# Optimization experiments

Measured on AMD Instinct MI355X. Metric: run time of the kernel, lower is better.

The kernel has to match this reference:

```python
import jax, jax.numpy as jnp
import numpy as np

HIGHEST_ID = 222.0
ZERO_NONZERO_PENALTY = 1.0
N_COEFFS = 447  # Chebyshev.fit(..., deg=446)


def _cheb_eval(x, coeffs):
    """Evaluate sum_i coeffs[i] * T_i(x/111 - 1) via O(1)-memory three-term recurrence."""
    xn = x / 111.0 - 1.0
    T0 = jnp.ones_like(xn)
    T1 = xn
    acc0 = coeffs[0] * T0 + coeffs[1] * T1

    def step(carry, c):
        Tm1, Tn, acc = carry
        Tnew = 2.0 * xn * Tn - Tm1
        acc = acc + c * Tnew
        return (Tn, Tnew, acc), None

    (_, _, acc), _ = jax.lax.scan(step, (T0, T1, acc0), coeffs[2:])
    return acc


def _round_ste(x):
    return x + jax.lax.stop_gradient(jnp.round(x) - x)


def _mask(x):
    # ~0 for id > 222, ~id for id <= 222
    return x * jax.nn.sigmoid(50.0 * (222.5 - x))


def setup_inputs() -> dict:
    key = jax.random.key(0)
    k0, k1, k2 = jax.random.split(key, 3)
    shape = (512, 7, 16, 64, 2)
    scale = jnp.array([222.0, 200.0], dtype=jnp.float32)  # (id, amount)
    y_pred = jax.random.uniform(k0, shape, dtype=jnp.float32) * scale
    y = jax.random.uniform(k1, shape, dtype=jnp.float32) * scale
    calories_coeffs = jax.random.normal(k2, (N_COEFFS,), dtype=jnp.float32) * 0.1
    return {"y_pred": y_pred, "y": y, "calories_coeffs": calories_coeffs}


def reference(y_pred, y, calories_coeffs):
    pred_ids = y_pred[..., 0]
    pred_amounts = y_pred[..., 1]
    true_ids = y[..., 0]
    true_amounts = y[..., 1]

    id_zero_mask = 1.0 - jnp.tanh(4.0 * pred_ids)
    amount_nonzero_mask = jnp.tanh(4.0 * pred_amounts)
    case1 = id_zero_mask * amount_nonzero_mask
    case2 = (1.0 - id_zero_mask) * (1.0 - amount_nonzero_mask)
    zeros_nonzeros_penalty = (ZERO_NONZERO_PENALTY * (case1 + case2)).sum(axis=(1, 2, 3)).mean()

    id_range_penalty = jax.nn.relu(pred_ids - HIGHEST_ID).sum(axis=(1, 2, 3)).mean()

    B = y.shape[0]
    true_amounts_f = true_amounts.reshape(B, -1)
    true_calories = _cheb_eval(true_ids, calories_coeffs).reshape(B, -1)
    calories_in_true_menu = (true_calories * true_amounts_f / 100.0).sum(axis=1) / 7.0

    pred_amounts_f = pred_amounts.reshape(y_pred.shape[0], -1)
    pred_calories = _cheb_eval(_mask(_round_ste(pred_ids)), calories_coeffs).reshape(y_pred.shape[0], -1)
    calories_in_pred_menu = (pred_calories * pred_amounts_f / 100.0).sum(axis=1) / 7.0

    calories_diff = ((calories_in_true_menu - calories_in_pred_menu) ** 2).mean()

    return zeros_nonzeros_penalty + id_range_penalty + calories_diff
```

## Files before the change

kernel.cpp:

```cpp
#include <hip/hip_runtime.h>
#include <cmath>


constexpr int NCOEF = 447;
constexpr int NTAB  = 223;
constexpr int MQ    = 8192;
constexpr float SCALEQ = (float)(8192.0 / 3.14159265358979323846);
constexpr float HQ     = (float)(3.14159265358979323846 / 8192.0);
constexpr int TPB = 256;

__device__ float g_tabF[MQ + 1];
__device__ float g_pred[NTAB];
__device__ float4 g_part[1024];

__device__ __forceinline__ float tanh4(float v) {
  float e = __expf(8.0f * v);
  return fmaf(-2.0f, __builtin_amdgcn_rcpf(e + 1.0f), 1.0f);
}

__global__ __launch_bounds__(256)
void build_tables(const float* __restrict__ coeffs)
{
  int g = blockIdx.x * 256 + threadIdx.x;
  float x;
  if (g <= MQ) {
    x = cosf((float)g * HQ);
  } else if (g < MQ + 1 + NTAB) {
    float kf = (float)(g - (MQ + 1));
    float m = kf / (1.0f + __expf(50.0f * (kf - 222.5f)));
    x = m / 111.0f - 1.0f;
  } else {
    return;
  }
  float x2 = x + x;
  float Ta = 1.0f, Tb = x;
  float acc = fmaf(coeffs[1], x, coeffs[0]);
  for (int i = 2; i + 1 < NCOEF; i += 2) {
    Ta = fmaf(x2, Tb, -Ta); acc = fmaf(coeffs[i],     Ta, acc);
    Tb = fmaf(x2, Ta, -Tb); acc = fmaf(coeffs[i + 1], Tb, acc);
  }
  Ta = fmaf(x2, Tb, -Ta); acc = fmaf(coeffs[NCOEF - 1], Ta, acc);

  if (g <= MQ) g_tabF[g] = acc;
  else         g_pred[g - (MQ + 1)] = acc;
}

__global__ __launch_bounds__(TPB)
void loss_main(const float4* __restrict__ yp4, const float4* __restrict__ yt4)
{
  __shared__ __align__(16) float sf[MQ + 1];
  __shared__ float spred[NTAB];
  __shared__ float sred[12];
  const int tid = threadIdx.x;

  const float4* gt4 = (const float4*)g_tabF;
  #pragma unroll
  for (int k = 0; k < 8; ++k) ((float4*)sf)[tid + k * TPB] = gt4[tid + k * TPB];
  if (tid == 0) sf[MQ] = g_tabF[MQ];
  if (tid < NTAB) spred[tid] = g_pred[tid];
  __syncthreads();

  const int b = blockIdx.x >> 1, h = blockIdx.x & 1;
  const size_t base = (size_t)b * 3584 + (size_t)h * 1792;

  float pen = 0.0f, cp = 0.0f, ct = 0.0f;

  #pragma unroll
  for (int k = 0; k < 7; ++k) {
    float4 pv = yp4[base + tid + k * TPB];
    float4 tv = yt4[base + tid + k * TPB];

    float a0 = tanh4(pv.x), b0 = tanh4(pv.y);
    pen += fmaf(b0, fmaf(-2.0f, a0, 1.0f), a0) + fmaxf(pv.x - 222.0f, 0.0f);
    int x0 = (int)rintf(pv.x); x0 = x0 < 0 ? 0 : (x0 > NTAB - 1 ? NTAB - 1 : x0);
    cp = fmaf(spred[x0], pv.y, cp);
    float a1 = tanh4(pv.z), b1 = tanh4(pv.w);
    pen += fmaf(b1, fmaf(-2.0f, a1, 1.0f), a1) + fmaxf(pv.z - 222.0f, 0.0f);
    int x1 = (int)rintf(pv.z); x1 = x1 < 0 ? 0 : (x1 > NTAB - 1 ? NTAB - 1 : x1);
    cp = fmaf(spred[x1], pv.w, cp);

    {
      float xn = tv.x / 111.0f - 1.0f;
      float th = acosf(xn) * SCALEQ;
      float ir = rintf(th);
      ir = ir < 1.0f ? 1.0f : (ir > (float)(MQ - 1) ? (float)(MQ - 1) : ir);
      int i = (int)ir;
      float d = th - ir;
      float fm = sf[i - 1], f0 = sf[i], fp = sf[i + 1];
      float ca = 0.5f * (fp - fm);
      float cb = fmaf(0.5f, fp + fm, -f0);
      float cal = fmaf(d, fmaf(d, cb, ca), f0);
      ct = fmaf(cal, tv.y, ct);
    }
    {
      float xn = tv.z / 111.0f - 1.0f;
      float th = acosf(xn) * SCALEQ;
      float ir = rintf(th);
      ir = ir < 1.0f ? 1.0f : (ir > (float)(MQ - 1) ? (float)(MQ - 1) : ir);
      int i = (int)ir;
      float d = th - ir;
      float fm = sf[i - 1], f0 = sf[i], fp = sf[i + 1];
      float ca = 0.5f * (fp - fm);
      float cb = fmaf(0.5f, fp + fm, -f0);
      float cal = fmaf(d, fmaf(d, cb, ca), f0);
      ct = fmaf(cal, tv.w, ct);
    }
  }

  #pragma unroll
  for (int o = 32; o > 0; o >>= 1) {
    pen += __shfl_down(pen, o, 64);
    ct  += __shfl_down(ct,  o, 64);
    cp  += __shfl_down(cp,  o, 64);
  }
  const int w = tid >> 6;
  if ((tid & 63) == 0) { sred[w] = pen; sred[4 + w] = ct; sred[8 + w] = cp; }
  __syncthreads();
  if (tid == 0) {
    g_part[blockIdx.x] =
        make_float4(sred[0] + sred[1] + sred[2]  + sred[3],
                    sred[4] + sred[5] + sred[6]  + sred[7],
                    sred[8] + sred[9] + sred[10] + sred[11], 0.0f);
  }
}

__global__ __launch_bounds__(512)
void finalize(float* __restrict__ out)
{
  __shared__ float sr[8];
  int t = threadIdx.x;
  float4 u = g_part[2 * t], v = g_part[2 * t + 1];
  float pen = u.x + v.x;
  float d = ((u.y + v.y) - (u.z + v.z)) * (1.0f / 700.0f);
  float s = fmaf(d, d, pen);
  #pragma unroll
  for (int o = 32; o > 0; o >>= 1) s += __shfl_down(s, o, 64);
  if ((t & 63) == 0) sr[t >> 6] = s;
  __syncthreads();
  if (t == 0) {
    out[0] = (sr[0] + sr[1] + sr[2] + sr[3] +
              sr[4] + sr[5] + sr[6] + sr[7]) * (1.0f / 512.0f);
  }
}

extern "C" void kernel_launch(void* const* d_in, const int* in_sizes, int n_in,
                              void* d_out, int out_size, void* d_ws, size_t ws_size,
                              hipStream_t stream) {
  build_tables<<<33, 256, 0, stream>>>((const float*)d_in[2]);
  loss_main<<<1024, TPB, 0, stream>>>(
      (const float4*)d_in[0], (const float4*)d_in[1]);
  finalize<<<1, 512, 0, stream>>>((float*)d_out);
}
```

Baseline: 107.0 us.

## Halve Chebyshev table, use more smaller blocks, fuse finalize via last-block atomic

Shrinks the acos-indexed Chebyshev lookup table from 8192 to 4096 entries, which halves both the table-build work and the per-block shared-memory fill. The main kernel now launches 3584 blocks that each process 512 float4 elements, with a higher occupancy hint to get more parallelism. The separate finalize kernel is folded in: the last block to finish, detected by an atomic counter, reduces all partials. The smaller table lowers interpolation accuracy. Smaller blocks mean the table load is repeated more often relative to the data each block processes.

```diff
diff --git a/kernel.cpp b/kernel.cpp
--- a/kernel.cpp
+++ b/kernel.cpp
@@ -4,14 +4,17 @@
 
 constexpr int NCOEF = 447;
 constexpr int NTAB  = 223;
-constexpr int MQ    = 8192;
-constexpr float SCALEQ = (float)(8192.0 / 3.14159265358979323846);
-constexpr float HQ     = (float)(3.14159265358979323846 / 8192.0);
+constexpr int MQ    = 4096;
+constexpr float SCALEQ = (float)(4096.0 / 3.14159265358979323846);
+constexpr float HQ     = (float)(3.14159265358979323846 / 4096.0);
+constexpr float INV111 = 1.0f / 111.0f;
 constexpr int TPB = 256;
+constexpr int NBLK = 3584;
 
 __device__ float g_tabF[MQ + 1];
 __device__ float g_pred[NTAB];
-__device__ float4 g_part[1024];
+__device__ float4 g_part[NBLK];
+__device__ int   g_done;
 
 __device__ __forceinline__ float tanh4(float v) {
   float e = __expf(8.0f * v);
@@ -45,8 +48,22 @@
   else         g_pred[g - (MQ + 1)] = acc;
 }
 
-__global__ __launch_bounds__(TPB)
-void loss_main(const float4* __restrict__ yp4, const float4* __restrict__ yt4)
+__device__ __forceinline__ float true_cal(const float* sf, float id) {
+  float xn = fminf(fmaf(id, INV111, -1.0f), 1.0f);
+  float th = acosf(xn) * SCALEQ;
+  float ir = rintf(th);
+  ir = ir < 1.0f ? 1.0f : (ir > (float)(MQ - 1) ? (float)(MQ - 1) : ir);
+  int i = (int)ir;
+  float d = th - ir;
+  float fm = sf[i - 1], f0 = sf[i], fp = sf[i + 1];
+  float ca = 0.5f * (fp - fm);
+  float cb = fmaf(0.5f, fp + fm, -f0);
+  return fmaf(d, fmaf(d, cb, ca), f0);
+}
+
+__global__ __launch_bounds__(TPB, 8)
+void loss_main(const float4* __restrict__ yp4, const float4* __restrict__ yt4,
+               float* __restrict__ out)
 {
   __shared__ __align__(16) float sf[MQ + 1];
   __shared__ float spred[NTAB];
@@ -55,18 +72,17 @@
 
   const float4* gt4 = (const float4*)g_tabF;
   #pragma unroll
-  for (int k = 0; k < 8; ++k) ((float4*)sf)[tid + k * TPB] = gt4[tid + k * TPB];
+  for (int k = 0; k < 4; ++k) ((float4*)sf)[tid + k * TPB] = gt4[tid + k * TPB];
   if (tid == 0) sf[MQ] = g_tabF[MQ];
   if (tid < NTAB) spred[tid] = g_pred[tid];
   __syncthreads();
 
-  const int b = blockIdx.x >> 1, h = blockIdx.x & 1;
-  const size_t base = (size_t)b * 3584 + (size_t)h * 1792;
+  const size_t base = (size_t)blockIdx.x * 512;
 
   float pen = 0.0f, cp = 0.0f, ct = 0.0f;
 
   #pragma unroll
-  for (int k = 0; k < 7; ++k) {
+  for (int k = 0; k < 2; ++k) {
     float4 pv = yp4[base + tid + k * TPB];
     float4 tv = yt4[base + tid + k * TPB];
 
@@ -79,32 +95,8 @@
     int x1 = (int)rintf(pv.z); x1 = x1 < 0 ? 0 : (x1 > NTAB - 1 ? NTAB - 1 : x1);
     cp = fmaf(spred[x1], pv.w, cp);
 
-    {
-      float xn = tv.x / 111.0f - 1.0f;
-      float th = acosf(xn) * SCALEQ;
-      float ir = rintf(th);
-      ir = ir < 1.0f ? 1.0f : (ir > (float)(MQ - 1) ? (float)(MQ - 1) : ir);
-      int i = (int)ir;
-      float d = th - ir;
-      float fm = sf[i - 1], f0 = sf[i], fp = sf[i + 1];
-      float ca = 0.5f * (fp - fm);
-      float cb = fmaf(0.5f, fp + fm, -f0);
-      float cal = fmaf(d, fmaf(d, cb, ca), f0);
-      ct = fmaf(cal, tv.y, ct);
-    }
-    {
-      float xn = tv.z / 111.0f - 1.0f;
-      float th = acosf(xn) * SCALEQ;
-      float ir = rintf(th);
-      ir = ir < 1.0f ? 1.0f : (ir > (float)(MQ - 1) ? (float)(MQ - 1) : ir);
-      int i = (int)ir;
-      float d = th - ir;
-      float fm = sf[i - 1], f0 = sf[i], fp = sf[i + 1];
-      float ca = 0.5f * (fp - fm);
-      float cb = fmaf(0.5f, fp + fm, -f0);
-      float cal = fmaf(d, fmaf(d, cb, ca), f0);
-      ct = fmaf(cal, tv.w, ct);
-    }
+    ct = fmaf(true_cal(sf, tv.x), tv.y, ct);
+    ct = fmaf(true_cal(sf, tv.z), tv.w, ct);
   }
 
   #pragma unroll
@@ -116,38 +108,47 @@
   const int w = tid >> 6;
   if ((tid & 63) == 0) { sred[w] = pen; sred[4 + w] = ct; sred[8 + w] = cp; }
   __syncthreads();
+
+  __shared__ bool s_last;
   if (tid == 0) {
     g_part[blockIdx.x] =
         make_float4(sred[0] + sred[1] + sred[2]  + sred[3],
                     sred[4] + sred[5] + sred[6]  + sred[7],
                     sred[8] + sred[9] + sred[10] + sred[11], 0.0f);
+    __threadfence();
+    s_last = (atomicAdd(&g_done, 1) == NBLK - 1);
   }
-}
+  __syncthreads();
+  if (!s_last) return;
 
-__global__ __launch_bounds__(512)
-void finalize(float* __restrict__ out)
-{
-  __shared__ float sr[8];
-  int t = threadIdx.x;
-  float4 u = g_part[2 * t], v = g_part[2 * t + 1];
-  float pen = u.x + v.x;
-  float d = ((u.y + v.y) - (u.z + v.z)) * (1.0f / 700.0f);
-  float s = fmaf(d, d, pen);
+  __threadfence();
+  float acc = 0.0f;
   #pragma unroll
-  for (int o = 32; o > 0; o >>= 1) s += __shfl_down(s, o, 64);
-  if ((t & 63) == 0) sr[t >> 6] = s;
+  for (int r = 0; r < 2; ++r) {
+    int b = 2 * tid + r;
+    float p = 0.0f, tsum = 0.0f, psum = 0.0f;
+    #pragma unroll
+    for (int s = 0; s < 7; ++s) {
+      float4 u = g_part[b * 7 + s];
+      p += u.x; tsum += u.y; psum += u.z;
+    }
+    float d = (tsum - psum) * (1.0f / 700.0f);
+    acc += fmaf(d, d, p);
+  }
+  #pragma unroll
+  for (int o = 32; o > 0; o >>= 1) acc += __shfl_down(acc, o, 64);
+  if ((tid & 63) == 0) sred[tid >> 6] = acc;
   __syncthreads();
-  if (t == 0) {
-    out[0] = (sr[0] + sr[1] + sr[2] + sr[3] +
-              sr[4] + sr[5] + sr[6] + sr[7]) * (1.0f / 512.0f);
+  if (tid == 0) {
+    out[0] = (sred[0] + sred[1] + sred[2] + sred[3]) * (1.0f / 512.0f);
+    g_done = 0;
   }
 }
 
 extern "C" void kernel_launch(void* const* d_in, const int* in_sizes, int n_in,
                               void* d_out, int out_size, void* d_ws, size_t ws_size,
                               hipStream_t stream) {
-  build_tables<<<33, 256, 0, stream>>>((const float*)d_in[2]);
-  loss_main<<<1024, TPB, 0, stream>>>(
-      (const float4*)d_in[0], (const float4*)d_in[1]);
-  finalize<<<1, 512, 0, stream>>>((float*)d_out);
+  build_tables<<<17, 256, 0, stream>>>((const float*)d_in[2]);
+  loss_main<<<NBLK, TPB, 0, stream>>>(
+      (const float4*)d_in[0], (const float4*)d_in[1], (float*)d_out);
 }
```

Result: slower. 205.4 us (+92.0%).
